# Optimization experiments

Measured on AMD Instinct MI355X. Metric: run time of the kernel, lower is better.

Reference implementation:

```python
import jax, jax.numpy as jnp
import numpy as np

BATCH = 1024
SEQ = 512
HID = 512
OUT = 10


def setup_inputs() -> dict:
    key = jax.random.key(0)
    k1, k2, k3, k4 = jax.random.split(key, 4)
    # Xavier-ish scaled params (scale irrelevant for correctness baseline)
    x = jax.random.normal(k1, (BATCH, SEQ), dtype=jnp.float32)
    W_hx = jax.random.normal(k2, (HID, 1), dtype=jnp.float32) * (1.0 / np.sqrt(1 + HID)).astype(np.float32)
    W_hh = jax.random.normal(k3, (HID, HID), dtype=jnp.float32) * (1.0 / np.sqrt(2 * HID)).astype(np.float32)
    W_yh = jax.random.normal(k4, (OUT, HID), dtype=jnp.float32) * (1.0 / np.sqrt(HID + OUT)).astype(np.float32)
    b_h = jnp.zeros((HID, 1), dtype=jnp.float32)
    b_y = jnp.zeros((OUT, 1), dtype=jnp.float32)
    return {"x": x, "W_hx": W_hx, "W_hh": W_hh, "W_yh": W_yh, "b_h": b_h, "b_y": b_y}


def reference(x, W_hx, W_hh, W_yh, b_h, b_y):
    # x: [B, T]; hidden state h: [H, B] (column-major layout as in the torch code)
    B = x.shape[0]
    H = W_hh.shape[0]
    xs = x.T  # [T, B], scan over time

    def step(h, x_t):
        # x_t: [B] -> treated as [1, B]; W_hx: [H, 1]
        h_new = jnp.tanh(W_hx @ x_t[None, :] + W_hh @ h + b_h)  # [H, B]
        return h_new, None

    h0 = jnp.zeros((H, B), dtype=x.dtype)
    h_T, _ = jax.lax.scan(step, h0, xs)
    y = W_yh @ h_T + b_y  # [O, B] — only the last timestep's output is returned
    return y.T  # [B, O]
```

## Files before the change

### kernel.cpp

```cpp
#include <hip/hip_runtime.h>


#define BATCH 1024
#define SEQT  512
#define HID   512
#define OUTD  10
#define KR    12
#define NKK   16

typedef _Float16 f16;
typedef _Float16 f16x8 __attribute__((ext_vector_type(8)));
typedef _Float16 f16x4 __attribute__((ext_vector_type(4)));
typedef float    f32x4 __attribute__((ext_vector_type(4)));

__global__ void wconv_kernel(const float* __restrict__ Whh, f16* __restrict__ frag) {
    int id = blockIdx.x * blockDim.x + threadIdx.x;
    int lane = id & 63;
    int kk   = (id >> 6) & 15;
    int mt   = (id >> 10) & 3;
    int g    = id >> 12;
    int m = g * 64 + mt * 16 + (lane & 15);
    int k = kk * 32 + ((lane >> 4) & 3) * 8;
    const float* src = Whh + (size_t)m * HID + k;
    f16x8 v;
#pragma unroll
    for (int j = 0; j < 8; ++j) v[j] = (f16)src[j];
    *(f16x8*)(frag + (size_t)id * 8) = v;
}

__device__ __forceinline__ float fast_tanh(float v) {
    v = fminf(fmaxf(v, -15.f), 15.f);
    float e = __expf(2.f * v);
    return (e - 1.f) * __builtin_amdgcn_rcpf(e + 1.f);
}

__global__ __launch_bounds__(512)
__attribute__((amdgpu_waves_per_eu(2, 2)))
void rnn_cu(
    const f16* __restrict__ frag,
    const float* __restrict__ x,
    const float* __restrict__ Whx,
    const float* __restrict__ bh,
    const float* __restrict__ Wyh,
    const float* __restrict__ by,
    float* __restrict__ out)
{
    __shared__ f16 HB[8192];
    __shared__ f16 WL[65536];

    const int tid  = threadIdx.x;
    const int w    = tid >> 6;
    const int lane = tid & 63;
    const int n    = lane & 15;
    const int q    = lane >> 4;
    const int bg   = blockIdx.x;

    {
        f16x8 z;
#pragma unroll
        for (int j = 0; j < 8; ++j) z[j] = (f16)0.f;
        *(f16x8*)&HB[tid * 16]     = z;
        *(f16x8*)&HB[tid * 16 + 8] = z;
    }

    const f16x8* A = (const f16x8*)frag;

#pragma unroll
    for (int mt = 0; mt < 4; ++mt)
#pragma unroll
        for (int kkl = 0; kkl < 4; ++kkl) {
            int e = ((w * 4 + mt) * 4 + kkl) * 64 + lane;
            *(f16x8*)&WL[e * 8] = A[((w * 4 + mt) * 16 + (KR + kkl)) * 64 + lane];
        }

    f16x8 Wr[KR * 4];
#pragma unroll
    for (int kk = 0; kk < KR; ++kk)
#pragma unroll
        for (int mt = 0; mt < 4; ++mt)
            Wr[kk * 4 + mt] = A[((w * 4 + mt) * 16 + kk) * 64 + lane];

    __syncthreads();

    const int b = bg * 16 + n;
    const float* xp = x + (size_t)b * SEQT;

#pragma unroll 1
    for (int s = 0; s < SEQT; ++s) {
        float xv = xp[s];

        f32x4 acc[4] = {{0,0,0,0},{0,0,0,0},{0,0,0,0},{0,0,0,0}};

#pragma unroll
        for (int t = 0; t < NKK; ++t) {
            constexpr int ord[NKK] = {12, 0, 1, 2, 13, 3, 4, 5,
                                      14, 6, 7, 8, 15, 9, 10, 11};
            const int kb = ord[t];
            f16x8 bf = *(const f16x8*)&HB[(kb * 64 + lane) * 8];
            if ((t & 3) == 0) {
                const int kkl = t >> 2;
#pragma unroll
                for (int mt = 0; mt < 4; ++mt) {
                    f16x8 a = *(const f16x8*)&WL[(((w * 4 + mt) * 4 + kkl) * 64 + lane) * 8];
                    acc[mt] = __builtin_amdgcn_mfma_f32_16x16x32_f16(
                        a, bf, acc[mt], 0, 0, 0);
                }
            } else {
                const int rb = t - 1 - (t >> 2);
#pragma unroll
                for (int mt = 0; mt < 4; ++mt)
                    acc[mt] = __builtin_amdgcn_mfma_f32_16x16x32_f16(
                        Wr[rb * 4 + mt], bf, acc[mt], 0, 0, 0);
            }
        }

        __syncthreads();

        const float* wbp = Whx;
        const float* bbp = bh;
        asm volatile("" : "+v"(wbp), "+v"(bbp));

#pragma unroll
        for (int mt = 0; mt < 4; ++mt) {
            int m0 = w * 64 + mt * 16 + q * 4;
            f32x4 whx4 = *(const f32x4*)(wbp + m0);
            f32x4 bh4  = *(const f32x4*)(bbp + m0);
            f16x4 hv;
#pragma unroll
            for (int r = 0; r < 4; ++r) {
                float pre = acc[mt][r] + whx4[r] * xv + bh4[r];
                hv[r] = (f16)fast_tanh(pre);
            }
            int kkd = w * 2 + (mt >> 1);
            int q2  = (mt & 1) * 2 + (q >> 1);
            int j0  = (q & 1) * 4;
            *(f16x4*)&HB[(kkd * 64 + q2 * 16 + n) * 8 + j0] = hv;
        }

        __syncthreads();
    }

    if (tid < 16 * OUTD) {
        const int nn = tid & 15;
        const int o  = tid >> 4;
        const float* wrow = Wyh + (size_t)o * HID;
        float sum = by[o];
        for (int kk = 0; kk < 16; ++kk)
#pragma unroll
            for (int q2 = 0; q2 < 4; ++q2) {
                f16x8 hv = *(const f16x8*)&HB[((kk * 64 + q2 * 16 + nn)) * 8];
                const float* wp = wrow + kk * 32 + q2 * 8;
#pragma unroll
                for (int j = 0; j < 8; ++j) sum += wp[j] * (float)hv[j];
            }
        out[(size_t)(bg * 16 + nn) * OUTD + o] = sum;
    }
}

extern "C" void kernel_launch(void* const* d_in, const int* in_sizes, int n_in,
                              void* d_out, int out_size, void* d_ws, size_t ws_size,
                              hipStream_t stream) {
    const float* x   = (const float*)d_in[0];
    const float* Whx = (const float*)d_in[1];
    const float* Whh = (const float*)d_in[2];
    const float* Wyh = (const float*)d_in[3];
    const float* bh  = (const float*)d_in[4];
    const float* by  = (const float*)d_in[5];
    float* out = (float*)d_out;

    char* ws   = (char*)d_ws;
    f16*  frag = (f16*)(ws + (1 << 20));

    wconv_kernel<<<128, 256, 0, stream>>>(Whh, frag);
    rnn_cu<<<64, 512, 0, stream>>>(frag, x, Whx, bh, Wyh, by, out);
}
```

Baseline: 1.126 ms.

## Double-buffer hidden state to drop one barrier per step and fuse weight conversion

The hidden-state buffer in LDS is doubled so each timestep reads one buffer and writes the other. This removes the barrier between the MFMA reads and the tanh writeback, leaving one __syncthreads per step. The separate fp32-to-fp16 weight fragment conversion kernel is also removed: each block now loads and converts its W_hh fragments straight from global memory. That saves a launch and a round trip through the workspace, but every block repeats the conversion and LDS use grows by 16 KB.

```diff
diff --git a/kernel.cpp b/kernel.cpp
--- a/kernel.cpp
+++ b/kernel.cpp
@@ -13,31 +13,30 @@
 typedef _Float16 f16x4 __attribute__((ext_vector_type(4)));
 typedef float    f32x4 __attribute__((ext_vector_type(4)));
 
-__global__ void wconv_kernel(const float* __restrict__ Whh, f16* __restrict__ frag) {
-    int id = blockIdx.x * blockDim.x + threadIdx.x;
-    int lane = id & 63;
-    int kk   = (id >> 6) & 15;
-    int mt   = (id >> 10) & 3;
-    int g    = id >> 12;
-    int m = g * 64 + mt * 16 + (lane & 15);
-    int k = kk * 32 + ((lane >> 4) & 3) * 8;
-    const float* src = Whh + (size_t)m * HID + k;
-    f16x8 v;
-#pragma unroll
-    for (int j = 0; j < 8; ++j) v[j] = (f16)src[j];
-    *(f16x8*)(frag + (size_t)id * 8) = v;
-}
-
 __device__ __forceinline__ float fast_tanh(float v) {
     v = fminf(fmaxf(v, -15.f), 15.f);
     float e = __expf(2.f * v);
     return (e - 1.f) * __builtin_amdgcn_rcpf(e + 1.f);
 }
 
+__device__ __forceinline__ f16x8 ldfrag(const float* __restrict__ Whh,
+                                        int m, int k) {
+    const float* src = Whh + (size_t)m * HID + k;
+    f32x4 lo = *(const f32x4*)src;
+    f32x4 hi = *(const f32x4*)(src + 4);
+    f16x8 v;
+#pragma unroll
+    for (int j = 0; j < 4; ++j) {
+        v[j]     = (f16)lo[j];
+        v[4 + j] = (f16)hi[j];
+    }
+    return v;
+}
+
 __global__ __launch_bounds__(512)
 __attribute__((amdgpu_waves_per_eu(2, 2)))
 void rnn_cu(
-    const f16* __restrict__ frag,
+    const float* __restrict__ Whh,
     const float* __restrict__ x,
     const float* __restrict__ Whx,
     const float* __restrict__ bh,
@@ -45,7 +44,7 @@
     const float* __restrict__ by,
     float* __restrict__ out)
 {
-    __shared__ f16 HB[8192];
+    __shared__ f16 HB[2][8192];
     __shared__ f16 WL[65536];
 
     const int tid  = threadIdx.x;
@@ -59,18 +58,20 @@
         f16x8 z;
 #pragma unroll
         for (int j = 0; j < 8; ++j) z[j] = (f16)0.f;
-        *(f16x8*)&HB[tid * 16]     = z;
-        *(f16x8*)&HB[tid * 16 + 8] = z;
+        *(f16x8*)&HB[0][tid * 16]     = z;
+        *(f16x8*)&HB[0][tid * 16 + 8] = z;
     }
 
-    const f16x8* A = (const f16x8*)frag;
+    const int mbase = w * 64 + (lane & 15);
+    const int kcol  = ((lane >> 4) & 3) * 8;
 
 #pragma unroll
     for (int mt = 0; mt < 4; ++mt)
 #pragma unroll
         for (int kkl = 0; kkl < 4; ++kkl) {
             int e = ((w * 4 + mt) * 4 + kkl) * 64 + lane;
-            *(f16x8*)&WL[e * 8] = A[((w * 4 + mt) * 16 + (KR + kkl)) * 64 + lane];
+            *(f16x8*)&WL[e * 8] =
+                ldfrag(Whh, mbase + mt * 16, (KR + kkl) * 32 + kcol);
         }
 
     f16x8 Wr[KR * 4];
@@ -78,7 +79,7 @@
     for (int kk = 0; kk < KR; ++kk)
 #pragma unroll
         for (int mt = 0; mt < 4; ++mt)
-            Wr[kk * 4 + mt] = A[((w * 4 + mt) * 16 + kk) * 64 + lane];
+            Wr[kk * 4 + mt] = ldfrag(Whh, mbase + mt * 16, kk * 32 + kcol);
 
     __syncthreads();
 
@@ -87,6 +88,8 @@
 
 #pragma unroll 1
     for (int s = 0; s < SEQT; ++s) {
+        const f16* hbr = &HB[s & 1][0];
+        f16*       hbw = &HB[(s & 1) ^ 1][0];
         float xv = xp[s];
 
         f32x4 acc[4] = {{0,0,0,0},{0,0,0,0},{0,0,0,0},{0,0,0,0}};
@@ -96,7 +99,7 @@
             constexpr int ord[NKK] = {12, 0, 1, 2, 13, 3, 4, 5,
                                       14, 6, 7, 8, 15, 9, 10, 11};
             const int kb = ord[t];
-            f16x8 bf = *(const f16x8*)&HB[(kb * 64 + lane) * 8];
+            f16x8 bf = *(const f16x8*)&hbr[(kb * 64 + lane) * 8];
             if ((t & 3) == 0) {
                 const int kkl = t >> 2;
 #pragma unroll
@@ -114,7 +117,6 @@
             }
         }
 
-        __syncthreads();
 
         const float* wbp = Whx;
         const float* bbp = bh;
@@ -134,13 +136,14 @@
             int kkd = w * 2 + (mt >> 1);
             int q2  = (mt & 1) * 2 + (q >> 1);
             int j0  = (q & 1) * 4;
-            *(f16x4*)&HB[(kkd * 64 + q2 * 16 + n) * 8 + j0] = hv;
+            *(f16x4*)&hbw[(kkd * 64 + q2 * 16 + n) * 8 + j0] = hv;
         }
 
         __syncthreads();
     }
 
     if (tid < 16 * OUTD) {
+        const f16* hbT = &HB[SEQT & 1][0];
         const int nn = tid & 15;
         const int o  = tid >> 4;
         const float* wrow = Wyh + (size_t)o * HID;
@@ -148,7 +151,7 @@
         for (int kk = 0; kk < 16; ++kk)
 #pragma unroll
             for (int q2 = 0; q2 < 4; ++q2) {
-                f16x8 hv = *(const f16x8*)&HB[((kk * 64 + q2 * 16 + nn)) * 8];
+                f16x8 hv = *(const f16x8*)&hbT[((kk * 64 + q2 * 16 + nn)) * 8];
                 const float* wp = wrow + kk * 32 + q2 * 8;
 #pragma unroll
                 for (int j = 0; j < 8; ++j) sum += wp[j] * (float)hv[j];
@@ -168,9 +171,5 @@
     const float* by  = (const float*)d_in[5];
     float* out = (float*)d_out;
 
-    char* ws   = (char*)d_ws;
-    f16*  frag = (f16*)(ws + (1 << 20));
-
-    wconv_kernel<<<128, 256, 0, stream>>>(Whh, frag);
-    rnn_cu<<<64, 512, 0, stream>>>(frag, x, Whx, bh, Wyh, by, out);
+    rnn_cu<<<64, 512, 0, stream>>>(Whh, x, Whx, bh, Wyh, by, out);
 }
```

Result: slower. 1.185 ms (+5.2%).
